# Performance work log

Hardware: AMD Instinct MI355X
Metric: run time of the kernel (lower is better)

## Reference

```python
import jax, jax.numpy as jnp
import numpy as np

K_GAUSS = 10
HIDDEN = 512


def setup_inputs() -> dict:
    key = jax.random.key(0)
    k1, k2, k3 = jax.random.split(key, 3)
    lstm_out = jax.random.normal(k1, (16, 1024, HIDDEN), dtype=jnp.float32)
    char_seq = jax.random.uniform(k2, (16, 600, 80), dtype=jnp.float32)
    # Dense(3*k_gaussians): small init so exp(params) stays in a sane range
    W = jax.random.normal(k3, (HIDDEN, 3 * K_GAUSS), dtype=jnp.float32) * 0.02
    bias = jnp.zeros((3 * K_GAUSS,), dtype=jnp.float32)
    return {"lstm_out": lstm_out, "char_seq": char_seq, "W": W, "bias": bias}


def reference(lstm_out, char_seq, W, bias):
    # lstm_out: [B,T,H], char_seq: [B,U,A]
    U = char_seq.shape[1]
    params = jnp.einsum('bth,hp->btp', lstm_out, W) + bias  # [B,T,3K]
    exp_params = jnp.exp(params)
    a, b, k = jnp.split(exp_params, 3, axis=2)              # each [B,T,K]
    u = jnp.arange(U, dtype=lstm_out.dtype).reshape(1, 1, U, 1)  # char indices
    # gaussian mixture window weights phi[b,t,u] = sum_k a*exp(-b*(k-u)^2)
    gaussians = a[:, :, None, :] * jnp.exp(-b[:, :, None, :] * jnp.square(k[:, :, None, :] - u))  # [B,T,U,K]
    char_weights = jnp.sum(gaussians, axis=3)               # [B,T,U]
    # alphabet_window[b,t,a] = sum_u phi[b,t,u] * char_seq[b,u,a]
    return jnp.einsum('btu,bua->bta', char_weights, char_seq)
```

## Files before the change

kernel.cpp:

```cpp
#include <hip/hip_runtime.h>
#include <math.h>

#define BB 16
#define TD 1024
#define HD 512
#define UD 600
#define AD 80
#define KG 10
#define PC 30
#define PP 32

#define LOG2E 1.4426950408889634f

#if __has_builtin(__builtin_amdgcn_exp2f)
#define EXP2F(x) __builtin_amdgcn_exp2f(x)
#else
#define EXP2F(x) exp2f(x)
#endif

typedef short v8s __attribute__((ext_vector_type(8)));
typedef float v4f __attribute__((ext_vector_type(4)));

__device__ inline unsigned short f2bf(float f) {
    unsigned u = __float_as_uint(f);
    return (unsigned short)((u + 0x7FFF + ((u >> 16) & 1)) >> 16);
}

__global__ void k_wprep(const float* __restrict__ W,
                        unsigned short* __restrict__ Wfh,
                        unsigned short* __restrict__ Wfl) {
    int p = blockIdx.x * 256 + threadIdx.x;
    for (; p < 32768; p += 256 * 32) {
        int j = p & 7, l = (p >> 3) & 63, n = (p >> 9) & 1, kt = p >> 10;
        int k = kt * 32 + ((l >> 4) * 8) + j;
        int c = n * 16 + (l & 15);
        float v = (c < PC) ? W[k * PC + c] : 0.f;
        unsigned short h = f2bf(v);
        float hi_f = __uint_as_float(((unsigned)h) << 16);
        Wfh[p] = h;
        Wfl[p] = f2bf(v - hi_f);
    }
}

#define TT 32
#define UC 40
#define NCHUNK 15
#define NTHR 320

__global__ __launch_bounds__(NTHR) void k_fused(const float* __restrict__ x,
                                                const unsigned short* __restrict__ Wfh,
                                                const unsigned short* __restrict__ Wfl,
                                                const float* __restrict__ bias,
                                                const float* __restrict__ cs,
                                                float* __restrict__ out) {
    __shared__ float red[4 * TT * 33];
    __shared__ float params_l[TT * 36];
    __shared__ float cs_l[UC * AD];
    __shared__ float phi2[TT * 44];
    __shared__ float range_l[2];

    int tid = threadIdx.x;
    int b = blockIdx.y;
    int t0 = blockIdx.x * TT;
    long r0 = (long)b * TD + t0;

    int wv = tid >> 6;
    int l = tid & 63;
    int quad = l >> 4, m = l & 15;

    if (wv < 4) {
        v4f acc[2][2];
        #pragma unroll
        for (int mt = 0; mt < 2; mt++)
            #pragma unroll
            for (int n = 0; n < 2; n++)
                acc[mt][n] = (v4f){0.f, 0.f, 0.f, 0.f};

        #pragma unroll
        for (int kt = 0; kt < 4; kt++) {
            int g = wv * 4 + kt;
            v8s ah[2], al[2];
            #pragma unroll
            for (int mt = 0; mt < 2; mt++) {
                const float* xr = x + (r0 + mt * 16 + m) * HD + g * 32 + quad * 8;
                float4 xa = *(const float4*)(xr);
                float4 xb = *(const float4*)(xr + 4);
                float xf[8] = {xa.x, xa.y, xa.z, xa.w, xb.x, xb.y, xb.z, xb.w};
                #pragma unroll
                for (int j = 0; j < 8; j++) {
                    unsigned short h = f2bf(xf[j]);
                    ah[mt][j] = (short)h;
                    al[mt][j] = (short)f2bf(xf[j] - __uint_as_float(((unsigned)h) << 16));
                }
            }
            #pragma unroll
            for (int n = 0; n < 2; n++) {
                uint4 uh = *(const uint4*)&Wfh[((g * 2 + n) * 64 + l) * 8];
                uint4 ul = *(const uint4*)&Wfl[((g * 2 + n) * 64 + l) * 8];
                v8s bh, bl;
                __builtin_memcpy(&bh, &uh, 16);
                __builtin_memcpy(&bl, &ul, 16);
                #pragma unroll
                for (int mt = 0; mt < 2; mt++) {
                    acc[mt][n] = __builtin_amdgcn_mfma_f32_16x16x32_bf16(ah[mt], bh, acc[mt][n], 0, 0, 0);
                    acc[mt][n] = __builtin_amdgcn_mfma_f32_16x16x32_bf16(al[mt], bh, acc[mt][n], 0, 0, 0);
                    acc[mt][n] = __builtin_amdgcn_mfma_f32_16x16x32_bf16(ah[mt], bl, acc[mt][n], 0, 0, 0);
                }
            }
        }

        #pragma unroll
        for (int mt = 0; mt < 2; mt++)
            #pragma unroll
            for (int n = 0; n < 2; n++)
                #pragma unroll
                for (int r = 0; r < 4; r++)
                    red[wv * (TT * 33) + (mt * 16 + quad * 4 + r) * 33 + n * 16 + m]
                        = acc[mt][n][r];
    }
    __syncthreads();

    for (int idx = tid; idx < TT * PC; idx += NTHR) {
        int r = idx / PC, c = idx - r * PC;
        float s = red[0 * (TT * 33) + r * 33 + c] + red[1 * (TT * 33) + r * 33 + c]
                + red[2 * (TT * 33) + r * 33 + c] + red[3 * (TT * 33) + r * 33 + c];
        float e = __expf(s + bias[c]);
        params_l[r * 36 + c] = (c >= 10 && c < 20) ? (-e * LOG2E) : e;
    }
    __syncthreads();

    int tt = tid & 31;
    int sub = tid >> 5;
    float pa[KG], pnb[KG], pk[KG];
    #pragma unroll
    for (int q = 0; q < KG; q++) {
        pa[q]  = params_l[tt * 36 + q];
        pnb[q] = params_l[tt * 36 + 10 + q];
        pk[q]  = params_l[tt * 36 + 20 + q];
    }

    {
        float lo = 1e30f, hi = -1e30f;
        #pragma unroll
        for (int q = 0; q < KG; q++) {
            float bits = 46.f + fmaxf(0.f, __log2f(pa[q]));
            float w = __fsqrt_rn(bits / (-pnb[q]));
            lo = fminf(lo, pk[q] - w);
            hi = fmaxf(hi, pk[q] + w);
        }
        if (tid < 64) {
            #pragma unroll
            for (int mk = 1; mk < 64; mk <<= 1) {
                lo = fminf(lo, __shfl_xor(lo, mk));
                hi = fmaxf(hi, __shfl_xor(hi, mk));
            }
            if (tid == 0) { range_l[0] = lo; range_l[1] = hi; }
        }
    }
    __syncthreads();
    float lo_m = fminf(fmaxf(range_l[0], 0.f), (float)(UD - 1));
    float hi_m = fminf(fmaxf(range_l[1], 0.f), (float)(UD - 1));
    int ch_lo = (int)lo_m / UC;
    int ch_hi = (int)hi_m / UC;
    if (ch_lo > ch_hi) ch_lo = ch_hi;

    int tx = tid % 20;
    int ty = tid / 20;
    float4 acc0 = {0.f, 0.f, 0.f, 0.f};
    float4 acc1 = {0.f, 0.f, 0.f, 0.f};

    const float* csb = cs + (long)b * UD * AD;

    for (int ch = ch_lo; ch <= ch_hi; ch++) {
        int u0 = ch * UC;
        __syncthreads();

        for (int idx = tid; idx < (UC * AD) / 4; idx += NTHR) {
            *(float4*)&cs_l[idx * 4] = *(const float4*)&csb[u0 * AD + idx * 4];
        }

        float ph[4];
        #pragma unroll
        for (int i = 0; i < 4; i++) {
            float uf = (float)(u0 + sub * 4 + i);
            float ss = 0.f;
            #pragma unroll
            for (int q = 0; q < KG; q++) {
                float d = uf - pk[q];
                ss += pa[q] * EXP2F(pnb[q] * d * d);
            }
            ph[i] = ss;
        }
        *(float4*)&phi2[tt * 44 + sub * 4] = make_float4(ph[0], ph[1], ph[2], ph[3]);
        __syncthreads();

        #pragma unroll 2
        for (int g = 0; g < 10; g++) {
            float4 p0 = *(const float4*)&phi2[(ty * 2) * 44 + g * 4];
            float4 p1 = *(const float4*)&phi2[(ty * 2 + 1) * 44 + g * 4];
            #pragma unroll
            for (int i = 0; i < 4; i++) {
                float4 c4 = *(const float4*)&cs_l[(g * 4 + i) * AD + tx * 4];
                float pi0 = (i == 0) ? p0.x : (i == 1) ? p0.y : (i == 2) ? p0.z : p0.w;
                float pi1 = (i == 0) ? p1.x : (i == 1) ? p1.y : (i == 2) ? p1.z : p1.w;
                acc0.x += pi0 * c4.x; acc0.y += pi0 * c4.y;
                acc0.z += pi0 * c4.z; acc0.w += pi0 * c4.w;
                acc1.x += pi1 * c4.x; acc1.y += pi1 * c4.y;
                acc1.z += pi1 * c4.z; acc1.w += pi1 * c4.w;
            }
        }
    }

    long t = r0 + ty * 2;
    *(float4*)(out + t * AD + tx * 4) = acc0;
    *(float4*)(out + (t + 1) * AD + tx * 4) = acc1;
}

extern "C" void kernel_launch(void* const* d_in, const int* in_sizes, int n_in,
                              void* d_out, int out_size, void* d_ws, size_t ws_size,
                              hipStream_t stream) {
    const float* lstm = (const float*)d_in[0];
    const float* cs   = (const float*)d_in[1];
    const float* W    = (const float*)d_in[2];
    const float* bias = (const float*)d_in[3];
    float* out = (float*)d_out;

    unsigned short* Wfh = (unsigned short*)d_ws;
    unsigned short* Wfl = Wfh + 32768;

    k_wprep<<<32, 256, 0, stream>>>(W, Wfh, Wfl);
    dim3 grid(TD / TT, BB);
    k_fused<<<grid, NTHR, 0, stream>>>(lstm, Wfh, Wfl, bias, cs, out);
}
```

Before: 89.10 us.

## Halve time tile to 16 rows and prefetch first char chunk in idle wave

Shrinks the per-block time tile from 32 to 16 rows, doubling the grid and giving each thread one output row instead of two. It adds a min-blocks hint to launch bounds for higher occupancy. The otherwise idle fifth wave now loads the first char_seq chunk into shared memory while the other four waves run the MFMA projection, overlapping that load with compute. The trade-off is more blocks, each repeating the char_seq chunk loads and range computation, and less register reuse in the inner accumulation. It also relies on the chunk loop starting at chunk 0 whenever the prefetched buffer is used.

```diff
diff --git a/kernel.cpp b/kernel.cpp
--- a/kernel.cpp
+++ b/kernel.cpp
@@ -42,17 +42,17 @@
     }
 }
 
-#define TT 32
+#define TT 16
 #define UC 40
 #define NCHUNK 15
 #define NTHR 320
 
-__global__ __launch_bounds__(NTHR) void k_fused(const float* __restrict__ x,
-                                                const unsigned short* __restrict__ Wfh,
-                                                const unsigned short* __restrict__ Wfl,
-                                                const float* __restrict__ bias,
-                                                const float* __restrict__ cs,
-                                                float* __restrict__ out) {
+__global__ __launch_bounds__(NTHR, 4) void k_fused(const float* __restrict__ x,
+                                                   const unsigned short* __restrict__ Wfh,
+                                                   const unsigned short* __restrict__ Wfl,
+                                                   const float* __restrict__ bias,
+                                                   const float* __restrict__ cs,
+                                                   float* __restrict__ out) {
     __shared__ float red[4 * TT * 33];
     __shared__ float params_l[TT * 36];
     __shared__ float cs_l[UC * AD];
@@ -68,30 +68,24 @@
     int l = tid & 63;
     int quad = l >> 4, m = l & 15;
 
+    const float* csb = cs + (long)b * UD * AD;
+
     if (wv < 4) {
-        v4f acc[2][2];
-        #pragma unroll
-        for (int mt = 0; mt < 2; mt++)
-            #pragma unroll
-            for (int n = 0; n < 2; n++)
-                acc[mt][n] = (v4f){0.f, 0.f, 0.f, 0.f};
+        v4f acc[2] = {{0.f, 0.f, 0.f, 0.f}, {0.f, 0.f, 0.f, 0.f}};
 
         #pragma unroll
         for (int kt = 0; kt < 4; kt++) {
             int g = wv * 4 + kt;
-            v8s ah[2], al[2];
-            #pragma unroll
-            for (int mt = 0; mt < 2; mt++) {
-                const float* xr = x + (r0 + mt * 16 + m) * HD + g * 32 + quad * 8;
-                float4 xa = *(const float4*)(xr);
-                float4 xb = *(const float4*)(xr + 4);
-                float xf[8] = {xa.x, xa.y, xa.z, xa.w, xb.x, xb.y, xb.z, xb.w};
-                #pragma unroll
-                for (int j = 0; j < 8; j++) {
-                    unsigned short h = f2bf(xf[j]);
-                    ah[mt][j] = (short)h;
-                    al[mt][j] = (short)f2bf(xf[j] - __uint_as_float(((unsigned)h) << 16));
-                }
+            const float* xr = x + (r0 + m) * HD + g * 32 + quad * 8;
+            float4 xa = *(const float4*)(xr);
+            float4 xb = *(const float4*)(xr + 4);
+            float xf[8] = {xa.x, xa.y, xa.z, xa.w, xb.x, xb.y, xb.z, xb.w};
+            v8s ah, al;
+            #pragma unroll
+            for (int j = 0; j < 8; j++) {
+                unsigned short h = f2bf(xf[j]);
+                ah[j] = (short)h;
+                al[j] = (short)f2bf(xf[j] - __uint_as_float(((unsigned)h) << 16));
             }
             #pragma unroll
             for (int n = 0; n < 2; n++) {
@@ -100,23 +94,20 @@
                 v8s bh, bl;
                 __builtin_memcpy(&bh, &uh, 16);
                 __builtin_memcpy(&bl, &ul, 16);
-                #pragma unroll
-                for (int mt = 0; mt < 2; mt++) {
-                    acc[mt][n] = __builtin_amdgcn_mfma_f32_16x16x32_bf16(ah[mt], bh, acc[mt][n], 0, 0, 0);
-                    acc[mt][n] = __builtin_amdgcn_mfma_f32_16x16x32_bf16(al[mt], bh, acc[mt][n], 0, 0, 0);
-                    acc[mt][n] = __builtin_amdgcn_mfma_f32_16x16x32_bf16(ah[mt], bl, acc[mt][n], 0, 0, 0);
-                }
-            }
-        }
-
-        #pragma unroll
-        for (int mt = 0; mt < 2; mt++)
-            #pragma unroll
-            for (int n = 0; n < 2; n++)
-                #pragma unroll
-                for (int r = 0; r < 4; r++)
-                    red[wv * (TT * 33) + (mt * 16 + quad * 4 + r) * 33 + n * 16 + m]
-                        = acc[mt][n][r];
+                acc[n] = __builtin_amdgcn_mfma_f32_16x16x32_bf16(ah, bh, acc[n], 0, 0, 0);
+                acc[n] = __builtin_amdgcn_mfma_f32_16x16x32_bf16(al, bh, acc[n], 0, 0, 0);
+                acc[n] = __builtin_amdgcn_mfma_f32_16x16x32_bf16(ah, bl, acc[n], 0, 0, 0);
+            }
+        }
+
+        #pragma unroll
+        for (int n = 0; n < 2; n++)
+            #pragma unroll
+            for (int r = 0; r < 4; r++)
+                red[wv * (TT * 33) + (quad * 4 + r) * 33 + n * 16 + m] = acc[n][r];
+    } else {
+        for (int idx = l; idx < (UC * AD) / 4; idx += 64)
+            *(float4*)&cs_l[idx * 4] = *(const float4*)&csb[idx * 4];
     }
     __syncthreads();
 
@@ -129,8 +120,8 @@
     }
     __syncthreads();
 
-    int tt = tid & 31;
-    int sub = tid >> 5;
+    int tt = tid & 15;
+    int sub = tid >> 4;
     float pa[KG], pnb[KG], pk[KG];
     #pragma unroll
     for (int q = 0; q < KG; q++) {
@@ -167,22 +158,21 @@
     int tx = tid % 20;
     int ty = tid / 20;
     float4 acc0 = {0.f, 0.f, 0.f, 0.f};
-    float4 acc1 = {0.f, 0.f, 0.f, 0.f};
-
-    const float* csb = cs + (long)b * UD * AD;
 
     for (int ch = ch_lo; ch <= ch_hi; ch++) {
         int u0 = ch * UC;
         __syncthreads();
 
-        for (int idx = tid; idx < (UC * AD) / 4; idx += NTHR) {
-            *(float4*)&cs_l[idx * 4] = *(const float4*)&csb[u0 * AD + idx * 4];
-        }
-
-        float ph[4];
-        #pragma unroll
-        for (int i = 0; i < 4; i++) {
-            float uf = (float)(u0 + sub * 4 + i);
+        if (ch != 0) {
+            for (int idx = tid; idx < (UC * AD) / 4; idx += NTHR) {
+                *(float4*)&cs_l[idx * 4] = *(const float4*)&csb[u0 * AD + idx * 4];
+            }
+        }
+
+        float ph[2];
+        #pragma unroll
+        for (int i = 0; i < 2; i++) {
+            float uf = (float)(u0 + sub * 2 + i);
             float ss = 0.f;
             #pragma unroll
             for (int q = 0; q < KG; q++) {
@@ -191,29 +181,23 @@
             }
             ph[i] = ss;
         }
-        *(float4*)&phi2[tt * 44 + sub * 4] = make_float4(ph[0], ph[1], ph[2], ph[3]);
+        *(float2*)&phi2[tt * 44 + sub * 2] = make_float2(ph[0], ph[1]);
         __syncthreads();
 
         #pragma unroll 2
         for (int g = 0; g < 10; g++) {
-            float4 p0 = *(const float4*)&phi2[(ty * 2) * 44 + g * 4];
-            float4 p1 = *(const float4*)&phi2[(ty * 2 + 1) * 44 + g * 4];
+            float4 p0 = *(const float4*)&phi2[ty * 44 + g * 4];
             #pragma unroll
             for (int i = 0; i < 4; i++) {
                 float4 c4 = *(const float4*)&cs_l[(g * 4 + i) * AD + tx * 4];
                 float pi0 = (i == 0) ? p0.x : (i == 1) ? p0.y : (i == 2) ? p0.z : p0.w;
-                float pi1 = (i == 0) ? p1.x : (i == 1) ? p1.y : (i == 2) ? p1.z : p1.w;
                 acc0.x += pi0 * c4.x; acc0.y += pi0 * c4.y;
                 acc0.z += pi0 * c4.z; acc0.w += pi0 * c4.w;
-                acc1.x += pi1 * c4.x; acc1.y += pi1 * c4.y;
-                acc1.z += pi1 * c4.z; acc1.w += pi1 * c4.w;
-            }
-        }
-    }
-
-    long t = r0 + ty * 2;
-    *(float4*)(out + t * AD + tx * 4) = acc0;
-    *(float4*)(out + (t + 1) * AD + tx * 4) = acc1;
+            }
+        }
+    }
+
+    *(float4*)(out + (r0 + ty) * AD + tx * 4) = acc0;
 }
 
 extern "C" void kernel_launch(void* const* d_in, const int* in_sizes, int n_in,
```

New measurement: 89.60 us. No clear change (+0.6%).
